# Optimization experiments

Measured on AMD Instinct MI355X. Metric: run time of the kernel, lower is better.

Reference implementation:

```python
import jax, jax.numpy as jnp
import numpy as np

NUM_POINTS = 131072
NUM_RETAIN = 65536  # int(131072 * 0.5)


def setup_inputs() -> dict:
    key = jax.random.key(0)
    k1, k2 = jax.random.split(key)
    points = jax.random.normal(k1, (64, NUM_POINTS, 4), dtype=jnp.float32)
    dropout_weights = jax.random.normal(k2, (NUM_POINTS,), dtype=jnp.float32)
    return {"points": points, "dropout_weights": dropout_weights}


def reference(points, dropout_weights):
    # points: [B, N, C]; dropout_weights: [N]
    sampling_probs = jax.nn.softmax(dropout_weights)               # [N]
    sum_weights = jnp.sum(sampling_probs)                          # scalar (== 1 up to fp error)
    scale = sampling_probs / (sum_weights + 1e-6)                  # [N]
    downsampled = points * scale[None, :, None]                    # [B, N, C]
    # topk is identical across batch since probs are batch-independent
    _, indices = jax.lax.top_k(sampling_probs, NUM_RETAIN)         # sorted descending, like torch.topk
    return downsampled[:, indices, :]                              # [B, num_retain, C]
```

## Files before the change

### kernel.cpp

```cpp
#include <hip/hip_runtime.h>
#include <hip/hip_bf16.h>
#include <cstdint>

#define NPTS  131072
#define NRET  65536
#define NBAT  64
#define NBUCK (1 << 18)
#define BSH   14

__device__ __forceinline__ unsigned int desc_key(float w) {
    unsigned int b = __float_as_uint(w);
    unsigned int s = b ^ ((unsigned int)((int)b >> 31) | 0x80000000u);
    return ~s;
}

__global__ void k_zero(uint4* __restrict__ p) {
    int t = blockIdx.x * 256 + threadIdx.x;
    p[t] = make_uint4(0u, 0u, 0u, 0u);
}

__global__ void k_pmax(const float* __restrict__ w, float* __restrict__ pmax) {
    __shared__ float sm[256];
    int tid = threadIdx.x;
    float m = -3.402823466e38f;
    for (int i = blockIdx.x * 256 + tid; i < NPTS; i += gridDim.x * 256)
        m = fmaxf(m, w[i]);
    sm[tid] = m; __syncthreads();
    for (int off = 128; off > 0; off >>= 1) {
        if (tid < off) sm[tid] = fmaxf(sm[tid], sm[tid + off]);
        __syncthreads();
    }
    if (tid == 0) pmax[blockIdx.x] = sm[0];
}

__global__ void k_exp_sum(const float* __restrict__ w, const float* __restrict__ pmax,
                          float* __restrict__ e_out, float* __restrict__ bs) {
    __shared__ float smm[256];
    __shared__ float smr[256];
    int tid = threadIdx.x;
    smm[tid] = pmax[tid]; __syncthreads();
    for (int off = 128; off > 0; off >>= 1) {
        if (tid < off) smm[tid] = fmaxf(smm[tid], smm[tid + off]);
        __syncthreads();
    }
    float m = smm[0];
    int task = blockIdx.x * 256 + tid;
    int base = task >> 3;
    int k    = task & 7;
    const float* wp = w + (size_t)base * 128;
    float* ep = e_out + (size_t)base * 128;
    float r = 0.0f;
    #pragma unroll
    for (int i = 0; i < 128; i += 8) {
        float e = (float)exp((double)(wp[i + k] - m));
        ep[i + k] = e;
        r += e;
    }
    smr[tid] = r; __syncthreads();
    if (k == 0)
        bs[base] = ((smr[tid]+smr[tid+1])+(smr[tid+2]+smr[tid+3]))
                 + ((smr[tid+4]+smr[tid+5])+(smr[tid+6]+smr[tid+7]));
}

__global__ void k_tree(const float* __restrict__ bs, float* __restrict__ dst, int mode) {
    __shared__ float sm[1024];
    int tid = threadIdx.x;
    sm[tid] = bs[tid]; __syncthreads();
    for (int n = 512; n >= 1; n >>= 1) {
        float v = 0.0f;
        if (tid < n) v = sm[2*tid] + sm[2*tid+1];
        __syncthreads();
        if (tid < n) sm[tid] = v;
        __syncthreads();
    }
    if (tid == 0) dst[0] = mode ? (1.0f / (sm[0] + 1e-6f)) : sm[0];
}

__global__ void k_prob_hist_sum(float* __restrict__ probs, const float* __restrict__ scal,
                                unsigned int* __restrict__ hist, float* __restrict__ bs2) {
    __shared__ float smr[256];
    int tid = threadIdx.x;
    int task = blockIdx.x * 256 + tid;
    int base = task >> 3;
    int k    = task & 7;
    float* pp = probs + (size_t)base * 128;
    float Z = scal[1];
    float r = 0.0f;
    #pragma unroll
    for (int i = 0; i < 128; i += 8) {
        float pv = pp[i + k] / Z;
        pp[i + k] = pv;
        r += pv;
        atomicAdd(&hist[desc_key(pv) >> BSH], 1u);
    }
    smr[tid] = r; __syncthreads();
    if (k == 0)
        bs2[base] = ((smr[tid]+smr[tid+1])+(smr[tid+2]+smr[tid+3]))
                  + ((smr[tid+4]+smr[tid+5])+(smr[tid+6]+smr[tid+7]));
}

__global__ void k_scan_local(const unsigned int* __restrict__ hist,
                             unsigned int* __restrict__ local,
                             unsigned int* __restrict__ chunksum) {
    __shared__ unsigned int sm[256];
    int tid = threadIdx.x;
    int g0 = (blockIdx.x * 256 + tid) * 4;
    uint4 h = *(const uint4*)&hist[g0];
    unsigned int s = h.x + h.y + h.z + h.w;
    sm[tid] = s; __syncthreads();
    for (int off = 1; off < 256; off <<= 1) {
        unsigned int t = (tid >= off) ? sm[tid - off] : 0u;
        __syncthreads();
        sm[tid] += t;
        __syncthreads();
    }
    unsigned int excl = sm[tid] - s;
    uint4 o;
    o.x = excl; o.y = excl + h.x; o.z = o.y + h.y; o.w = o.z + h.z;
    *(uint4*)&local[g0] = o;
    if (tid == 255) chunksum[blockIdx.x] = sm[255];
}

__global__ void k_scan_chunk(const unsigned int* __restrict__ chunksum,
                             unsigned int* __restrict__ chunkoff) {
    __shared__ unsigned int sm[256];
    int tid = threadIdx.x;
    unsigned int v = chunksum[tid];
    sm[tid] = v; __syncthreads();
    for (int off = 1; off < 256; off <<= 1) {
        unsigned int t = (tid >= off) ? sm[tid - off] : 0u;
        __syncthreads();
        sm[tid] += t;
        __syncthreads();
    }
    chunkoff[tid] = sm[tid] - v;
}

__global__ void k_scatter(const float* __restrict__ probs,
                          const unsigned int* __restrict__ local,
                          const unsigned int* __restrict__ chunkoff,
                          unsigned int* __restrict__ cnt,
                          unsigned long long* __restrict__ bucketed) {
    int i = blockIdx.x * 256 + threadIdx.x;
    unsigned int d = desc_key(probs[i]);
    unsigned int b = d >> BSH;
    unsigned int base = chunkoff[b >> 10] + local[b];
    unsigned int off = atomicAdd(&cnt[b], 1u);
    bucketed[base + off] = ((unsigned long long)d << 17) | (unsigned int)i;
}

__global__ void k_rank(const unsigned long long* __restrict__ bucketed,
                       const unsigned int* __restrict__ hist,
                       const unsigned int* __restrict__ local,
                       const unsigned int* __restrict__ chunkoff,
                       const float* __restrict__ probs,
                       const float* __restrict__ scal,
                       uint2* __restrict__ ret_rs) {
    int p = blockIdx.x * 256 + threadIdx.x;
    unsigned long long kk = bucketed[p];
    unsigned int b = (unsigned int)(kk >> 31);
    unsigned int start = chunkoff[b >> 10] + local[b];
    unsigned int len = hist[b];
    unsigned int c = 0;
    for (unsigned int q = start; q < start + len; ++q)
        c += (bucketed[q] < kk) ? 1u : 0u;
    unsigned int rank = start + c;
    if (rank < NRET) {
        unsigned int i = (unsigned int)(kk & 0x1FFFFu);
        ret_rs[rank] = make_uint2(i, __float_as_uint(probs[i] * scal[2]));
    }
}

__global__ void k_gather(const float4* __restrict__ pts,
                         const uint2* __restrict__ ret_rs,
                         float4* __restrict__ out) {
    int j = blockIdx.x;
    int v = j & 7;
    int s = j >> 3;
    int b = v + ((s >> 5) << 3);
    int r0 = ((s & 31) << 11) + threadIdx.x;
    const float4* src = pts + (size_t)b * NPTS;
    float4* dst = out + (size_t)b * NRET;

    uint2 rs[8];
    #pragma unroll
    for (int k = 0; k < 8; ++k) rs[k] = ret_rs[r0 + (k << 8)];
    float4 val[8];
    #pragma unroll
    for (int k = 0; k < 8; ++k) val[k] = src[rs[k].x];
    #pragma unroll
    for (int k = 0; k < 8; ++k) {
        float sc = __uint_as_float(rs[k].y);
        val[k].x *= sc; val[k].y *= sc; val[k].z *= sc; val[k].w *= sc;
        dst[r0 + (k << 8)] = val[k];
    }
}

extern "C" void kernel_launch(void* const* d_in, const int* in_sizes, int n_in,
                              void* d_out, int out_size, void* d_ws, size_t ws_size,
                              hipStream_t stream) {
    const float* pts = (const float*)d_in[0];
    const float* w   = (const float*)d_in[1];
    float* out = (float*)d_out;

    char* ws = (char*)d_ws;
    unsigned int* hist      = (unsigned int*)(ws + 0);
    unsigned int* cnt       = (unsigned int*)(ws + (1 << 20));
    unsigned int* local     = (unsigned int*)(ws + (2 << 20));
    unsigned int* chunksum  = (unsigned int*)(ws + (3 << 20));
    unsigned int* chunkoff  = (unsigned int*)(ws + (3 << 20) + 4096);
    float*        pmax      = (float*)(ws + (3 << 20) + 8192);
    float*        scal      = (float*)(ws + (3 << 20) + 12288);
    float*        bs        = (float*)(ws + (3 << 20) + 16384);
    float*        bs2       = (float*)(ws + (3 << 20) + 24576);
    float*        probs     = (float*)(ws + (3 << 20) + (1 << 19));
    unsigned long long* bucketed = (unsigned long long*)(ws + (4 << 20));
    uint2*        ret_rs    = (uint2*)(ws + (5 << 20));

    k_zero          <<<512, 256, 0, stream>>>((uint4*)ws);
    k_pmax          <<<256, 256, 0, stream>>>(w, pmax);
    k_exp_sum       <<<32,  256, 0, stream>>>(w, pmax, probs, bs);
    k_tree          <<<1,  1024, 0, stream>>>(bs, &scal[1], 0);
    k_prob_hist_sum <<<32,  256, 0, stream>>>(probs, scal, hist, bs2);
    k_tree          <<<1,  1024, 0, stream>>>(bs2, &scal[2], 1);
    k_scan_local    <<<256, 256, 0, stream>>>(hist, local, chunksum);
    k_scan_chunk    <<<1,   256, 0, stream>>>(chunksum, chunkoff);
    k_scatter       <<<NPTS / 256, 256, 0, stream>>>(probs, local, chunkoff, cnt, bucketed);
    k_rank          <<<NPTS / 256, 256, 0, stream>>>(bucketed, hist, local, chunkoff,
                                                     probs, scal, ret_rs);
    k_gather        <<<2048, 256, 0, stream>>>((const float4*)pts, ret_rs, (float4*)out);
}
```

Measured before the change: 124.4 us.

## Fuse setup kernels and restructure gather to loop over batches per index

Merges the zero-fill and partial-max kernels into one launch, and folds the second sum tree plus its reciprocal into the chunk-scan kernel, removing two launches. The gather kernel now loads each retained index/scale pair once and loops over eight batches, software-prefetching the next batch's point. This cuts launch overhead and redundant index loads, but each thread now has fewer independent loads in flight, and the tree summation order for the normaliser changes slightly.

```diff
diff --git a/kernel.cpp b/kernel.cpp
--- a/kernel.cpp
+++ b/kernel.cpp
@@ -14,23 +14,21 @@
     return ~s;
 }
 
-__global__ void k_zero(uint4* __restrict__ p) {
-    int t = blockIdx.x * 256 + threadIdx.x;
-    p[t] = make_uint4(0u, 0u, 0u, 0u);
-}
-
-__global__ void k_pmax(const float* __restrict__ w, float* __restrict__ pmax) {
-    __shared__ float sm[256];
-    int tid = threadIdx.x;
-    float m = -3.402823466e38f;
-    for (int i = blockIdx.x * 256 + tid; i < NPTS; i += gridDim.x * 256)
-        m = fmaxf(m, w[i]);
-    sm[tid] = m; __syncthreads();
-    for (int off = 128; off > 0; off >>= 1) {
-        if (tid < off) sm[tid] = fmaxf(sm[tid], sm[tid + off]);
-        __syncthreads();
-    }
-    if (tid == 0) pmax[blockIdx.x] = sm[0];
+__global__ void k_zero_pmax(const float* __restrict__ w, uint4* __restrict__ zp,
+                            float* __restrict__ pmax) {
+    int j = blockIdx.x, tid = threadIdx.x;
+    zp[j * 256 + tid] = make_uint4(0u, 0u, 0u, 0u);
+    if (j < 256) {
+        __shared__ float sm[256];
+        int i = j * 256 + tid;
+        float m = fmaxf(w[i], w[i + 65536]);
+        sm[tid] = m; __syncthreads();
+        for (int off = 128; off > 0; off >>= 1) {
+            if (tid < off) sm[tid] = fmaxf(sm[tid], sm[tid + off]);
+            __syncthreads();
+        }
+        if (tid == 0) pmax[j] = sm[0];
+    }
 }
 
 __global__ void k_exp_sum(const float* __restrict__ w, const float* __restrict__ pmax,
@@ -62,7 +60,7 @@
                  + ((smr[tid+4]+smr[tid+5])+(smr[tid+6]+smr[tid+7]));
 }
 
-__global__ void k_tree(const float* __restrict__ bs, float* __restrict__ dst, int mode) {
+__global__ void k_tree(const float* __restrict__ bs, float* __restrict__ dst) {
     __shared__ float sm[1024];
     int tid = threadIdx.x;
     sm[tid] = bs[tid]; __syncthreads();
@@ -73,7 +71,7 @@
         if (tid < n) sm[tid] = v;
         __syncthreads();
     }
-    if (tid == 0) dst[0] = mode ? (1.0f / (sm[0] + 1e-6f)) : sm[0];
+    if (tid == 0) dst[0] = sm[0];
 }
 
 __global__ void k_prob_hist_sum(float* __restrict__ probs, const float* __restrict__ scal,
@@ -121,12 +119,18 @@
     if (tid == 255) chunksum[blockIdx.x] = sm[255];
 }
 
-__global__ void k_scan_chunk(const unsigned int* __restrict__ chunksum,
-                             unsigned int* __restrict__ chunkoff) {
+__global__ void k_scan_chunk_inv(const unsigned int* __restrict__ chunksum,
+                                 unsigned int* __restrict__ chunkoff,
+                                 const float* __restrict__ bs2,
+                                 float* __restrict__ inv_dst) {
     __shared__ unsigned int sm[256];
+    __shared__ float smf[256];
     int tid = threadIdx.x;
     unsigned int v = chunksum[tid];
-    sm[tid] = v; __syncthreads();
+    sm[tid] = v;
+    const float* b4 = bs2 + tid * 4;
+    smf[tid] = (b4[0] + b4[1]) + (b4[2] + b4[3]);
+    __syncthreads();
     for (int off = 1; off < 256; off <<= 1) {
         unsigned int t = (tid >= off) ? sm[tid - off] : 0u;
         __syncthreads();
@@ -134,6 +138,14 @@
         __syncthreads();
     }
     chunkoff[tid] = sm[tid] - v;
+    for (int n = 128; n >= 1; n >>= 1) {
+        float t = 0.0f;
+        if (tid < n) t = smf[2*tid] + smf[2*tid+1];
+        __syncthreads();
+        if (tid < n) smf[tid] = t;
+        __syncthreads();
+    }
+    if (tid == 0) inv_dst[0] = 1.0f / (smf[0] + 1e-6f);
 }
 
 __global__ void k_scatter(const float* __restrict__ probs,
@@ -177,22 +189,19 @@
     int j = blockIdx.x;
     int v = j & 7;
     int s = j >> 3;
-    int b = v + ((s >> 5) << 3);
-    int r0 = ((s & 31) << 11) + threadIdx.x;
-    const float4* src = pts + (size_t)b * NPTS;
-    float4* dst = out + (size_t)b * NRET;
-
-    uint2 rs[8];
+    int r = (s << 8) + threadIdx.x;
+    uint2 rs = ret_rs[r];
+    float sc = __uint_as_float(rs.y);
+    float4 val = pts[(size_t)v * NPTS + rs.x];
     #pragma unroll
-    for (int k = 0; k < 8; ++k) rs[k] = ret_rs[r0 + (k << 8)];
-    float4 val[8];
-    #pragma unroll
-    for (int k = 0; k < 8; ++k) val[k] = src[rs[k].x];
-    #pragma unroll
-    for (int k = 0; k < 8; ++k) {
-        float sc = __uint_as_float(rs[k].y);
-        val[k].x *= sc; val[k].y *= sc; val[k].z *= sc; val[k].w *= sc;
-        dst[r0 + (k << 8)] = val[k];
+    for (int bt = 0; bt < 8; ++bt) {
+        int b = v + (bt << 3);
+        float4 nxt;
+        if (bt < 7) nxt = pts[(size_t)(b + 8) * NPTS + rs.x];
+        float4 o;
+        o.x = val.x * sc; o.y = val.y * sc; o.z = val.z * sc; o.w = val.w * sc;
+        out[(size_t)b * NRET + r] = o;
+        val = nxt;
     }
 }
 
@@ -217,14 +226,12 @@
     unsigned long long* bucketed = (unsigned long long*)(ws + (4 << 20));
     uint2*        ret_rs    = (uint2*)(ws + (5 << 20));
 
-    k_zero          <<<512, 256, 0, stream>>>((uint4*)ws);
-    k_pmax          <<<256, 256, 0, stream>>>(w, pmax);
+    k_zero_pmax     <<<512, 256, 0, stream>>>(w, (uint4*)ws, pmax);
     k_exp_sum       <<<32,  256, 0, stream>>>(w, pmax, probs, bs);
-    k_tree          <<<1,  1024, 0, stream>>>(bs, &scal[1], 0);
+    k_tree          <<<1,  1024, 0, stream>>>(bs, &scal[1]);
     k_prob_hist_sum <<<32,  256, 0, stream>>>(probs, scal, hist, bs2);
-    k_tree          <<<1,  1024, 0, stream>>>(bs2, &scal[2], 1);
     k_scan_local    <<<256, 256, 0, stream>>>(hist, local, chunksum);
-    k_scan_chunk    <<<1,   256, 0, stream>>>(chunksum, chunkoff);
+    k_scan_chunk_inv<<<1,   256, 0, stream>>>(chunksum, chunkoff, bs2, &scal[2]);
     k_scatter       <<<NPTS / 256, 256, 0, stream>>>(probs, local, chunkoff, cnt, bucketed);
     k_rank          <<<NPTS / 256, 256, 0, stream>>>(bucketed, hist, local, chunkoff,
                                                      probs, scal, ret_rs);
```

Measured after the change: 150.1 us. 20.6% more time.
